# Kernel tuning notes

Hardware: AMD Instinct MI355X
Metric: run time of the kernel (lower is better)

Reference implementation:

```python
import jax, jax.numpy as jnp
import numpy as np

N = 100_000            # particles
E = 3_200_000          # edges (avg degree 32)
DIM = 3
H = 1.0                # kernel_radius
SIGMA = 3.0 / 359.0 / np.pi / H**3   # 3D quintic kernel normalization
RHO_REF = 1.0
P_REF = 100.0          # rho_ref * (10*u_ref)**2 / gamma, gamma=1
P_BG = 0.0             # p_bg_factor * p_ref
ETA0 = 0.01            # base_viscosity
EPS = 1e-8


def _qpows(d, p):
    q = d / H
    return (jnp.maximum(0.0, 1.0 - q) ** p,
            jnp.maximum(0.0, 2.0 - q) ** p,
            jnp.maximum(0.0, 3.0 - q) ** p)


def kernel_w(d):
    q1, q2, q3 = _qpows(d, 5)
    return SIGMA * (q3 - 6.0 * q2 + 15.0 * q1)


def kernel_grad_w(d):
    q1, q2, q3 = _qpows(d, 4)
    return (SIGMA / H) * (-5.0 * q3 + 30.0 * q2 - 75.0 * q1)


def setup_inputs() -> dict:
    key = jax.random.key(0)
    k1, k2, k3, k4 = jax.random.split(key, 4)
    r = jax.random.uniform(k1, (N, DIM), dtype=jnp.float32)   # positions in unit box
    v = jax.random.normal(k2, (N, DIM), dtype=jnp.float32)    # velocity history (last frame)
    i_s = jax.random.randint(k3, (E,), 0, N)                  # receivers
    j_s = jax.random.randint(k4, (E,), 0, N)                  # senders
    return {"r": r, "v": v, "i_s": i_s, "j_s": j_s}


def reference(r, v, i_s, j_s):
    n = r.shape[0]
    # --- per-edge gather + kernel ---
    dr = r[i_s] - r[j_s]                       # displacement_fn, [E,3]
    d = jnp.sqrt(jnp.sum(dr * dr, axis=-1))    # [E]
    w = kernel_w(d)
    # --- density summation (scatter) ---
    mass = jnp.ones((n,), r.dtype)
    rho = mass * jax.ops.segment_sum(w, i_s, num_segments=n)
    # Tait EoS, gamma=1
    p = P_REF * (rho / RHO_REF - 1.0) + P_BG
    eta = jnp.full((n,), ETA0, r.dtype)

    # --- per-edge acceleration (gather particle fields to edges) ---
    rho_i, rho_j = rho[i_s], rho[j_s]
    p_i, p_j = p[i_s], p[j_s]
    eta_i, eta_j = eta[i_s], eta[j_s]
    u_i, u_j = v[i_s], v[j_s]                  # u == v in _transform
    v_i, v_j = u_i, u_j

    eta_ij = 2.0 * eta_i * eta_j / (eta_i + eta_j + EPS)
    p_ij = (rho_j * p_i + rho_i * p_j) / (rho_i + rho_j)
    # ((m_i/rho_i)^2 + (m_j/rho_j)^2)/m_i with m == 1
    wvol = (1.0 / rho_i) ** 2 + (1.0 / rho_j) ** 2
    c = wvol * kernel_grad_w(d) / (d + EPS)    # [E]

    # transport stress A = (outer(rho_i*u_i, v_i-u_i) + outer(rho_j*u_j, v_j-u_j))/2, [E,3,3]
    A = 0.5 * (rho_i[:, None, None] * u_i[:, :, None] * (v_i - u_i)[:, None, :]
               + rho_j[:, None, None] * u_j[:, :, None] * (v_j - u_j)[:, None, :])
    Ar = jnp.einsum('eij,ej->ei', A, dr)

    a_eq_8 = c[:, None] * (-p_ij[:, None] * dr + Ar + eta_ij[:, None] * (u_i - u_j))
    p_bg_i = jnp.zeros_like(p_i)               # _transform passes zeros
    a_eq_13 = (c * p_bg_i)[:, None] * dr

    # --- scatter-reduce to particles ---
    dudt = jax.ops.segment_sum(a_eq_8, i_s, num_segments=n)   # [N,3]
    dvdt = jax.ops.segment_sum(a_eq_13, i_s, num_segments=n)  # [N,3]

    # pack state outputs: [rho, p, dudt(3), dvdt(3)] -> [N,8]
    return jnp.concatenate([rho[:, None], p[:, None], dudt, dvdt], axis=1)
```

## Files before the change

kernel.cpp:

```cpp
#include <hip/hip_runtime.h>
#include <math.h>

#ifndef M_PI
#define M_PI 3.14159265358979323846
#endif

static constexpr float kSigma = (float)(3.0 / 359.0 / M_PI);
static constexpr float kPRef  = 100.0f;
static constexpr float kEps   = 1e-8f;
static constexpr float kEta   = (float)(2.0 * 0.01 * 0.01 / (0.01 + 0.01 + 1e-8));

#define CHUNKA 2048

__device__ __forceinline__ float pow5f(float t) { float t2 = t * t; return t2 * t2 * t; }
__device__ __forceinline__ float pow4f(float t) { float t2 = t * t; return t2 * t2; }

__global__ void k_pack(const float* __restrict__ r, float4* __restrict__ pos4,
                       int* __restrict__ offset, int n, int E) {
    int i = blockIdx.x * blockDim.x + threadIdx.x;
    if (i == 0) offset[n] = E;
    if (i >= n) return;
    pos4[i] = make_float4(r[3 * i], r[3 * i + 1], r[3 * i + 2], 0.f);
}

__global__ void k_hist(const int* __restrict__ i_s, int* __restrict__ ghist,
                       int nbA, int nbins, int E, int shift) {
    __shared__ int h[512];
    int t = threadIdx.x, blk = blockIdx.x;
    for (int b = t; b < nbins; b += 256) h[b] = 0;
    __syncthreads();
    int base = blk * CHUNKA;
    int end = min(base + CHUNKA, E);
    for (int k = base + t; k < end; k += 256)
        atomicAdd(&h[i_s[k] >> shift], 1);
    __syncthreads();
    for (int b = t; b < nbins; b += 256)
        ghist[b * nbA + blk] = h[b];
}

__global__ void k_scan_block(const int* __restrict__ in, int* __restrict__ out,
                             int* __restrict__ bsum, int m) {
    __shared__ int s[256];
    int t = threadIdx.x;
    int i = blockIdx.x * 256 + t;
    int x = (i < m) ? in[i] : 0;
    s[t] = x;
    __syncthreads();
    for (int d = 1; d < 256; d <<= 1) {
        int v = (t >= d) ? s[t - d] : 0;
        __syncthreads();
        s[t] += v;
        __syncthreads();
    }
    if (i < m) out[i] = s[t] - x;
    if (t == 255) bsum[blockIdx.x] = s[255];
}

__global__ void k_scan_bsums(const int* __restrict__ bsum, int* __restrict__ bscan, int nb) {
    __shared__ int s[512];
    __shared__ int carry;
    int t = threadIdx.x;
    if (t == 0) carry = 0;
    __syncthreads();
    for (int base = 0; base < nb; base += 512) {
        int i = base + t;
        int x = (i < nb) ? bsum[i] : 0;
        s[t] = x;
        __syncthreads();
        for (int d = 1; d < 512; d <<= 1) {
            int v = (t >= d) ? s[t - d] : 0;
            __syncthreads();
            s[t] += v;
            __syncthreads();
        }
        if (i < nb) bscan[i] = s[t] - x + carry;
        __syncthreads();
        if (t == 511) carry += s[511];
        __syncthreads();
    }
}

__global__ void k_split(const int* __restrict__ i_s, const int* __restrict__ j_s,
                        const int* __restrict__ gscan, const int* __restrict__ bscan,
                        int* __restrict__ pairs, int nbA, int nbins, int E,
                        int shift, int jbits) {
    __shared__ int cur[512];
    int t = threadIdx.x, blk = blockIdx.x;
    for (int b = t; b < nbins; b += 256) {
        int idx = b * nbA + blk;
        cur[b] = gscan[idx] + bscan[idx >> 8];
    }
    __syncthreads();
    int fmask = (1 << shift) - 1;
    int base = blk * CHUNKA;
    int end = min(base + CHUNKA, E);
    for (int k = base + t; k < end; k += 256) {
        int i = i_s[k];
        int pos = atomicAdd(&cur[i >> shift], 1);
        pairs[pos] = ((i & fmask) << jbits) | j_s[k];
    }
}

__global__ void k_binsort(const int* __restrict__ pairs, const int* __restrict__ gscan,
                          const int* __restrict__ bscan, int* __restrict__ sortedJ,
                          int* __restrict__ offset, int nbA, int n, int E,
                          int shift, int jbits, int m) {
    __shared__ int h[512];
    __shared__ int sse[2];
    int b = blockIdx.x, t = threadIdx.x;
    int fine = 1 << shift;
    if (t < fine) h[t] = 0;
    if (t == 0) {
        int i0 = b * nbA;
        sse[0] = gscan[i0] + bscan[i0 >> 8];
        int i1 = (b + 1) * nbA;
        sse[1] = (i1 < m) ? (gscan[i1] + bscan[i1 >> 8]) : E;
    }
    __syncthreads();
    int s = sse[0], e = sse[1];
    int jm = (1 << jbits) - 1;
    for (int k = s + t; k < e; k += 512)
        atomicAdd(&h[pairs[k] >> jbits], 1);
    __syncthreads();
    int x = (t < fine) ? h[t] : 0;
    for (int d = 1; d < fine; d <<= 1) {
        int v = (t >= d && t < fine) ? h[t - d] : 0;
        __syncthreads();
        if (t < fine) h[t] += v;
        __syncthreads();
    }
    if (t < fine) {
        int i = (b << shift) + t;
        if (i < n) offset[i] = s + h[t] - x;
    }
    __syncthreads();
    if (t < fine) h[t] = s + h[t] - x;
    __syncthreads();
    for (int k = s + t; k < e; k += 512) {
        int pr = pairs[k];
        int pos = atomicAdd(&h[pr >> jbits], 1);
        sortedJ[pos] = pr & jm;
    }
}

__global__ void k_rho(const float4* __restrict__ pos4, const float* __restrict__ v,
                      const int* __restrict__ sortedJ, const int* __restrict__ offset,
                      float4* __restrict__ pv8, float* __restrict__ out, int n) {
    int p = (int)((blockIdx.x * (size_t)blockDim.x + threadIdx.x) >> 5);
    int lane = threadIdx.x & 31;
    if (p >= n) return;
    float4 ri = pos4[p];
    int s = offset[p], e = offset[p + 1];
    float acc = 0.f;
    for (int k = s + lane; k < e; k += 32) {
        int j = sortedJ[k];
        float4 rj = pos4[j];
        float dx = ri.x - rj.x, dy = ri.y - rj.y, dz = ri.z - rj.z;
        float d = sqrtf(dx * dx + dy * dy + dz * dz);
        float t1 = fmaxf(1.f - d, 0.f);
        float t2 = fmaxf(2.f - d, 0.f);
        float t3 = fmaxf(3.f - d, 0.f);
        acc += kSigma * (pow5f(t3) - 6.f * pow5f(t2) + 15.f * pow5f(t1));
    }
    for (int o = 16; o; o >>= 1) acc += __shfl_down(acc, o, 32);
    if (lane == 0) {
        float rh = acc;
        float pp = kPRef * (rh - 1.0f);
        pv8[2 * p]     = make_float4(ri.x, ri.y, ri.z, rh);
        pv8[2 * p + 1] = make_float4(v[3 * p], v[3 * p + 1], v[3 * p + 2], pp);
        float* o = out + (size_t)p * 8;
        o[0] = rh;
        o[1] = pp;
        o[5] = 0.f; o[6] = 0.f; o[7] = 0.f;
    }
}

__global__ void k_acc(const float4* __restrict__ pv8, const int* __restrict__ sortedJ,
                      const int* __restrict__ offset, float* __restrict__ out, int n) {
    int p = (int)((blockIdx.x * (size_t)blockDim.x + threadIdx.x) >> 5);
    int lane = threadIdx.x & 31;
    if (p >= n) return;
    float4 ai = pv8[2 * p], bi = pv8[2 * p + 1];
    float rho_i = ai.w, p_i = bi.w;
    float inv_i = 1.0f / rho_i;
    float inv2_i = inv_i * inv_i;
    int s = offset[p], e = offset[p + 1];
    float ax = 0.f, ay = 0.f, az = 0.f;
    for (int k = s + lane; k < e; k += 32) {
        int j = sortedJ[k];
        float4 aj = pv8[2 * j];
        float4 bj = pv8[2 * j + 1];
        float rho_j = aj.w, p_j = bj.w;
        float dx = ai.x - aj.x, dy = ai.y - aj.y, dz = ai.z - aj.z;
        float d = sqrtf(dx * dx + dy * dy + dz * dz);
        float t1 = fmaxf(1.f - d, 0.f);
        float t2 = fmaxf(2.f - d, 0.f);
        float t3 = fmaxf(3.f - d, 0.f);
        float gw = kSigma * (-5.f * pow4f(t3) + 30.f * pow4f(t2) - 75.f * pow4f(t1));
        float inv_j = 1.0f / rho_j;
        float c = (inv2_i + inv_j * inv_j) * gw / (d + kEps);
        float p_ij = (rho_j * p_i + rho_i * p_j) / (rho_i + rho_j);
        ax += c * (kEta * (bi.x - bj.x) - p_ij * dx);
        ay += c * (kEta * (bi.y - bj.y) - p_ij * dy);
        az += c * (kEta * (bi.z - bj.z) - p_ij * dz);
    }
    for (int o = 16; o; o >>= 1) {
        ax += __shfl_down(ax, o, 32);
        ay += __shfl_down(ay, o, 32);
        az += __shfl_down(az, o, 32);
    }
    if (lane == 0) {
        float* o = out + (size_t)p * 8 + 2;
        o[0] = ax; o[1] = ay; o[2] = az;
    }
}

static inline char* wcarve(char*& ws, size_t bytes) {
    char* p = ws;
    ws += (bytes + 255) & ~(size_t)255;
    return p;
}

extern "C" void kernel_launch(void* const* d_in, const int* in_sizes, int n_in,
                              void* d_out, int out_size, void* d_ws, size_t ws_size,
                              hipStream_t stream) {
    const float* r = (const float*)d_in[0];
    const float* v = (const float*)d_in[1];
    const int* i_s = (const int*)d_in[2];
    const int* j_s = (const int*)d_in[3];
    int n = in_sizes[0] / 3;
    int E = in_sizes[2];
    float* out = (float*)d_out;

    int shift = 8;
    int nbins = ((n - 1) >> shift) + 1;
    while (nbins > 512) { shift++; nbins = ((n - 1) >> shift) + 1; }
    int jbits = 1;
    while ((1 << jbits) < n) jbits++;

    int nbA = (E + CHUNKA - 1) / CHUNKA;
    int m = nbins * nbA;
    int nb2 = (m + 255) / 256;

    char* ws = (char*)d_ws;
    float4* pos4   = (float4*)wcarve(ws, (size_t)n * 16);
    float4* pv8    = (float4*)wcarve(ws, (size_t)n * 32);
    int*    offset = (int*)wcarve(ws, (size_t)(n + 1) * 4);
    int*    ghist  = (int*)wcarve(ws, (size_t)m * 4);
    int*    gscan  = (int*)wcarve(ws, (size_t)m * 4);
    int*    bsum   = (int*)wcarve(ws, (size_t)nb2 * 4);
    int*    bscan  = (int*)wcarve(ws, (size_t)nb2 * 4);
    int*    pairs  = (int*)wcarve(ws, (size_t)E * 4);
    int*    sortedJ= (int*)wcarve(ws, (size_t)E * 4);

    const int bs = 256;
    int gn = (n + bs - 1) / bs;
    int gp = (n + 7) / 8;

    k_pack<<<gn, bs, 0, stream>>>(r, pos4, offset, n, E);
    k_hist<<<nbA, 256, 0, stream>>>(i_s, ghist, nbA, nbins, E, shift);
    k_scan_block<<<nb2, 256, 0, stream>>>(ghist, gscan, bsum, m);
    k_scan_bsums<<<1, 512, 0, stream>>>(bsum, bscan, nb2);
    k_split<<<nbA, 256, 0, stream>>>(i_s, j_s, gscan, bscan, pairs, nbA, nbins, E, shift, jbits);
    k_binsort<<<nbins, 512, 0, stream>>>(pairs, gscan, bscan, sortedJ, offset, nbA, n, E, shift, jbits, m);
    k_rho<<<gp, bs, 0, stream>>>(pos4, v, sortedJ, offset, pv8, out, n);
    k_acc<<<gp, bs, 0, stream>>>(pv8, sortedJ, offset, out, n);
}
```

Before: 214.6 us.

## Drop fine per-particle sort; accumulate per coarse bin with shared-memory atomics

Removes the second-level bin sort and the sortedJ/offset arrays. The density and acceleration kernels now run one 1024-thread block per coarse bin of 256 particles, reading that bin's unsorted pairs and summing into per-particle shared-memory slots with atomics instead of warp reductions over CSR segments. Histogram chunks grow to 8192 edges with 512-thread blocks. This saves a full pass over the edges plus the scatter write, at the cost of LDS float atomic contention and only about 391 large blocks, which may leave part of the device idle.

```diff
diff --git a/kernel.cpp b/kernel.cpp
--- a/kernel.cpp
+++ b/kernel.cpp
@@ -10,15 +10,13 @@
 static constexpr float kEps   = 1e-8f;
 static constexpr float kEta   = (float)(2.0 * 0.01 * 0.01 / (0.01 + 0.01 + 1e-8));
 
-#define CHUNKA 2048
+#define CHUNKA 8192
 
 __device__ __forceinline__ float pow5f(float t) { float t2 = t * t; return t2 * t2 * t; }
 __device__ __forceinline__ float pow4f(float t) { float t2 = t * t; return t2 * t2; }
 
-__global__ void k_pack(const float* __restrict__ r, float4* __restrict__ pos4,
-                       int* __restrict__ offset, int n, int E) {
+__global__ void k_pack(const float* __restrict__ r, float4* __restrict__ pos4, int n) {
     int i = blockIdx.x * blockDim.x + threadIdx.x;
-    if (i == 0) offset[n] = E;
     if (i >= n) return;
     pos4[i] = make_float4(r[3 * i], r[3 * i + 1], r[3 * i + 2], 0.f);
 }
@@ -27,14 +25,14 @@
                        int nbA, int nbins, int E, int shift) {
     __shared__ int h[512];
     int t = threadIdx.x, blk = blockIdx.x;
-    for (int b = t; b < nbins; b += 256) h[b] = 0;
+    for (int b = t; b < nbins; b += 512) h[b] = 0;
     __syncthreads();
     int base = blk * CHUNKA;
     int end = min(base + CHUNKA, E);
-    for (int k = base + t; k < end; k += 256)
+    for (int k = base + t; k < end; k += 512)
         atomicAdd(&h[i_s[k] >> shift], 1);
     __syncthreads();
-    for (int b = t; b < nbins; b += 256)
+    for (int b = t; b < nbins; b += 512)
         ghist[b * nbA + blk] = h[b];
 }
 
@@ -86,7 +84,7 @@
                         int shift, int jbits) {
     __shared__ int cur[512];
     int t = threadIdx.x, blk = blockIdx.x;
-    for (int b = t; b < nbins; b += 256) {
+    for (int b = t; b < nbins; b += 512) {
         int idx = b * nbA + blk;
         cur[b] = gscan[idx] + bscan[idx >> 8];
     }
@@ -94,22 +92,29 @@
     int fmask = (1 << shift) - 1;
     int base = blk * CHUNKA;
     int end = min(base + CHUNKA, E);
-    for (int k = base + t; k < end; k += 256) {
+    for (int k = base + t; k < end; k += 512) {
         int i = i_s[k];
         int pos = atomicAdd(&cur[i >> shift], 1);
         pairs[pos] = ((i & fmask) << jbits) | j_s[k];
     }
 }
 
-__global__ void k_binsort(const int* __restrict__ pairs, const int* __restrict__ gscan,
-                          const int* __restrict__ bscan, int* __restrict__ sortedJ,
-                          int* __restrict__ offset, int nbA, int n, int E,
+__global__ void k_rho_bin(const float4* __restrict__ pos4, const float* __restrict__ v,
+                          const int* __restrict__ pairs, const int* __restrict__ gscan,
+                          const int* __restrict__ bscan, float4* __restrict__ pv8,
+                          float* __restrict__ out, int nbA, int n, int E,
                           int shift, int jbits, int m) {
-    __shared__ int h[512];
+    __shared__ float srho[512];
+    __shared__ float4 spos[512];
     __shared__ int sse[2];
     int b = blockIdx.x, t = threadIdx.x;
-    int fine = 1 << shift;
-    if (t < fine) h[t] = 0;
+    int slots = 1 << shift;
+    int lo = b << shift;
+    for (int s0 = t; s0 < slots; s0 += 1024) {
+        srho[s0] = 0.f;
+        int i = lo + s0;
+        spos[s0] = (i < n) ? pos4[i] : make_float4(0.f, 0.f, 0.f, 0.f);
+    }
     if (t == 0) {
         int i0 = b * nbA;
         sse[0] = gscan[i0] + bscan[i0 >> 8];
@@ -119,77 +124,67 @@
     __syncthreads();
     int s = sse[0], e = sse[1];
     int jm = (1 << jbits) - 1;
-    for (int k = s + t; k < e; k += 512)
-        atomicAdd(&h[pairs[k] >> jbits], 1);
-    __syncthreads();
-    int x = (t < fine) ? h[t] : 0;
-    for (int d = 1; d < fine; d <<= 1) {
-        int v = (t >= d && t < fine) ? h[t - d] : 0;
-        __syncthreads();
-        if (t < fine) h[t] += v;
-        __syncthreads();
-    }
-    if (t < fine) {
-        int i = (b << shift) + t;
-        if (i < n) offset[i] = s + h[t] - x;
-    }
-    __syncthreads();
-    if (t < fine) h[t] = s + h[t] - x;
-    __syncthreads();
-    for (int k = s + t; k < e; k += 512) {
+    for (int k = s + t; k < e; k += 1024) {
         int pr = pairs[k];
-        int pos = atomicAdd(&h[pr >> jbits], 1);
-        sortedJ[pos] = pr & jm;
-    }
-}
-
-__global__ void k_rho(const float4* __restrict__ pos4, const float* __restrict__ v,
-                      const int* __restrict__ sortedJ, const int* __restrict__ offset,
-                      float4* __restrict__ pv8, float* __restrict__ out, int n) {
-    int p = (int)((blockIdx.x * (size_t)blockDim.x + threadIdx.x) >> 5);
-    int lane = threadIdx.x & 31;
-    if (p >= n) return;
-    float4 ri = pos4[p];
-    int s = offset[p], e = offset[p + 1];
-    float acc = 0.f;
-    for (int k = s + lane; k < e; k += 32) {
-        int j = sortedJ[k];
+        int slot = pr >> jbits, j = pr & jm;
         float4 rj = pos4[j];
+        float4 ri = spos[slot];
         float dx = ri.x - rj.x, dy = ri.y - rj.y, dz = ri.z - rj.z;
         float d = sqrtf(dx * dx + dy * dy + dz * dz);
         float t1 = fmaxf(1.f - d, 0.f);
         float t2 = fmaxf(2.f - d, 0.f);
         float t3 = fmaxf(3.f - d, 0.f);
-        acc += kSigma * (pow5f(t3) - 6.f * pow5f(t2) + 15.f * pow5f(t1));
-    }
-    for (int o = 16; o; o >>= 1) acc += __shfl_down(acc, o, 32);
-    if (lane == 0) {
-        float rh = acc;
+        float w = kSigma * (pow5f(t3) - 6.f * pow5f(t2) + 15.f * pow5f(t1));
+        atomicAdd(&srho[slot], w);
+    }
+    __syncthreads();
+    for (int s0 = t; s0 < slots; s0 += 1024) {
+        int i = lo + s0;
+        if (i >= n) continue;
+        float rh = srho[s0];
         float pp = kPRef * (rh - 1.0f);
-        pv8[2 * p]     = make_float4(ri.x, ri.y, ri.z, rh);
-        pv8[2 * p + 1] = make_float4(v[3 * p], v[3 * p + 1], v[3 * p + 2], pp);
-        float* o = out + (size_t)p * 8;
+        float4 sp = spos[s0];
+        pv8[2 * i]     = make_float4(sp.x, sp.y, sp.z, rh);
+        pv8[2 * i + 1] = make_float4(v[3 * i], v[3 * i + 1], v[3 * i + 2], pp);
+        float* o = out + (size_t)i * 8;
         o[0] = rh;
         o[1] = pp;
         o[5] = 0.f; o[6] = 0.f; o[7] = 0.f;
     }
 }
 
-__global__ void k_acc(const float4* __restrict__ pv8, const int* __restrict__ sortedJ,
-                      const int* __restrict__ offset, float* __restrict__ out, int n) {
-    int p = (int)((blockIdx.x * (size_t)blockDim.x + threadIdx.x) >> 5);
-    int lane = threadIdx.x & 31;
-    if (p >= n) return;
-    float4 ai = pv8[2 * p], bi = pv8[2 * p + 1];
-    float rho_i = ai.w, p_i = bi.w;
-    float inv_i = 1.0f / rho_i;
-    float inv2_i = inv_i * inv_i;
-    int s = offset[p], e = offset[p + 1];
-    float ax = 0.f, ay = 0.f, az = 0.f;
-    for (int k = s + lane; k < e; k += 32) {
-        int j = sortedJ[k];
+__global__ void k_acc_bin(const float4* __restrict__ pv8, const int* __restrict__ pairs,
+                          const int* __restrict__ gscan, const int* __restrict__ bscan,
+                          float* __restrict__ out, int nbA, int n, int E,
+                          int shift, int jbits, int m) {
+    __shared__ float sax[512], say[512], saz[512];
+    __shared__ float4 sab[1024];
+    __shared__ int sse[2];
+    int b = blockIdx.x, t = threadIdx.x;
+    int slots = 1 << shift;
+    int lo = b << shift;
+    for (int s0 = t; s0 < slots; s0 += 1024) { sax[s0] = 0.f; say[s0] = 0.f; saz[s0] = 0.f; }
+    for (int q = t; q < 2 * slots; q += 1024) {
+        int gi = 2 * lo + q;
+        sab[q] = (gi < 2 * n) ? pv8[gi] : make_float4(0.f, 0.f, 0.f, 0.f);
+    }
+    if (t == 0) {
+        int i0 = b * nbA;
+        sse[0] = gscan[i0] + bscan[i0 >> 8];
+        int i1 = (b + 1) * nbA;
+        sse[1] = (i1 < m) ? (gscan[i1] + bscan[i1 >> 8]) : E;
+    }
+    __syncthreads();
+    int s = sse[0], e = sse[1];
+    int jm = (1 << jbits) - 1;
+    for (int k = s + t; k < e; k += 1024) {
+        int pr = pairs[k];
+        int slot = pr >> jbits, j = pr & jm;
         float4 aj = pv8[2 * j];
         float4 bj = pv8[2 * j + 1];
+        float4 ai = sab[2 * slot];
+        float4 bi = sab[2 * slot + 1];
+        float rho_i = ai.w, p_i = bi.w;
         float rho_j = aj.w, p_j = bj.w;
         float dx = ai.x - aj.x, dy = ai.y - aj.y, dz = ai.z - aj.z;
         float d = sqrtf(dx * dx + dy * dy + dz * dz);
@@ -197,21 +192,19 @@
         float t2 = fmaxf(2.f - d, 0.f);
         float t3 = fmaxf(3.f - d, 0.f);
         float gw = kSigma * (-5.f * pow4f(t3) + 30.f * pow4f(t2) - 75.f * pow4f(t1));
-        float inv_j = 1.0f / rho_j;
-        float c = (inv2_i + inv_j * inv_j) * gw / (d + kEps);
+        float inv_i = 1.0f / rho_i, inv_j = 1.0f / rho_j;
+        float c = (inv_i * inv_i + inv_j * inv_j) * gw / (d + kEps);
         float p_ij = (rho_j * p_i + rho_i * p_j) / (rho_i + rho_j);
-        ax += c * (kEta * (bi.x - bj.x) - p_ij * dx);
-        ay += c * (kEta * (bi.y - bj.y) - p_ij * dy);
-        az += c * (kEta * (bi.z - bj.z) - p_ij * dz);
-    }
-    for (int o = 16; o; o >>= 1) {
-        ax += __shfl_down(ax, o, 32);
-        ay += __shfl_down(ay, o, 32);
-        az += __shfl_down(az, o, 32);
-    }
-    if (lane == 0) {
-        float* o = out + (size_t)p * 8 + 2;
-        o[0] = ax; o[1] = ay; o[2] = az;
+        atomicAdd(&sax[slot], c * (kEta * (bi.x - bj.x) - p_ij * dx));
+        atomicAdd(&say[slot], c * (kEta * (bi.y - bj.y) - p_ij * dy));
+        atomicAdd(&saz[slot], c * (kEta * (bi.z - bj.z) - p_ij * dz));
+    }
+    __syncthreads();
+    for (int s0 = t; s0 < slots; s0 += 1024) {
+        int i = lo + s0;
+        if (i >= n) continue;
+        float* o = out + (size_t)i * 8 + 2;
+        o[0] = sax[s0]; o[1] = say[s0]; o[2] = saz[s0];
     }
 }
 
@@ -243,26 +236,22 @@
     int nb2 = (m + 255) / 256;
 
     char* ws = (char*)d_ws;
-    float4* pos4   = (float4*)wcarve(ws, (size_t)n * 16);
-    float4* pv8    = (float4*)wcarve(ws, (size_t)n * 32);
-    int*    offset = (int*)wcarve(ws, (size_t)(n + 1) * 4);
-    int*    ghist  = (int*)wcarve(ws, (size_t)m * 4);
-    int*    gscan  = (int*)wcarve(ws, (size_t)m * 4);
-    int*    bsum   = (int*)wcarve(ws, (size_t)nb2 * 4);
-    int*    bscan  = (int*)wcarve(ws, (size_t)nb2 * 4);
-    int*    pairs  = (int*)wcarve(ws, (size_t)E * 4);
-    int*    sortedJ= (int*)wcarve(ws, (size_t)E * 4);
+    float4* pos4  = (float4*)wcarve(ws, (size_t)n * 16);
+    float4* pv8   = (float4*)wcarve(ws, (size_t)n * 32);
+    int*    ghist = (int*)wcarve(ws, (size_t)m * 4);
+    int*    gscan = (int*)wcarve(ws, (size_t)m * 4);
+    int*    bsum  = (int*)wcarve(ws, (size_t)nb2 * 4);
+    int*    bscan = (int*)wcarve(ws, (size_t)nb2 * 4);
+    int*    pairs = (int*)wcarve(ws, (size_t)E * 4);
 
     const int bs = 256;
     int gn = (n + bs - 1) / bs;
-    int gp = (n + 7) / 8;
-
-    k_pack<<<gn, bs, 0, stream>>>(r, pos4, offset, n, E);
-    k_hist<<<nbA, 256, 0, stream>>>(i_s, ghist, nbA, nbins, E, shift);
+
+    k_pack<<<gn, bs, 0, stream>>>(r, pos4, n);
+    k_hist<<<nbA, 512, 0, stream>>>(i_s, ghist, nbA, nbins, E, shift);
     k_scan_block<<<nb2, 256, 0, stream>>>(ghist, gscan, bsum, m);
     k_scan_bsums<<<1, 512, 0, stream>>>(bsum, bscan, nb2);
-    k_split<<<nbA, 256, 0, stream>>>(i_s, j_s, gscan, bscan, pairs, nbA, nbins, E, shift, jbits);
-    k_binsort<<<nbins, 512, 0, stream>>>(pairs, gscan, bscan, sortedJ, offset, nbA, n, E, shift, jbits, m);
-    k_rho<<<gp, bs, 0, stream>>>(pos4, v, sortedJ, offset, pv8, out, n);
-    k_acc<<<gp, bs, 0, stream>>>(pv8, sortedJ, offset, out, n);
-}
+    k_split<<<nbA, 512, 0, stream>>>(i_s, j_s, gscan, bscan, pairs, nbA, nbins, E, shift, jbits);
+    k_rho_bin<<<nbins, 1024, 0, stream>>>(pos4, v, pairs, gscan, bscan, pv8, out, nbA, n, E, shift, jbits, m);
+    k_acc_bin<<<nbins, 1024, 0, stream>>>(pv8, pairs, gscan, bscan, out, nbA, n, E, shift, jbits, m);
+}
```

Result: no change. 214.5 us (-0.1%).
